# Kernel tuning notes

Measured on AMD Instinct MI355X. Metric: run time of the kernel, lower is better.

The kernel has to match this reference:

```python
import jax, jax.numpy as jnp
import numpy as np
import math

QUERY_DIM = 1024
KEY_DIM = 768
VALUE_DIM = 768
NUM_HEADS = 16
HEAD_DIM = QUERY_DIM // NUM_HEADS


def setup_inputs() -> dict:
    key = jax.random.key(0)
    ks = jax.random.split(key, 11)
    B, Sq, Skv = 4, 2048, 2048
    query = jax.random.normal(ks[0], (B, Sq, QUERY_DIM), dtype=jnp.float32)
    k_in = jax.random.normal(ks[1], (B, Skv, KEY_DIM), dtype=jnp.float32)
    v_in = jax.random.normal(ks[2], (B, Skv, VALUE_DIM), dtype=jnp.float32)
    # Linear weights stored as [in, out] (y = x @ W + b), equivalent to torch's x @ W^T.
    def lin(k, fan_in, fan_out):
        bound = 1.0 / math.sqrt(fan_in)
        kw, kb = jax.random.split(k)
        W = jax.random.uniform(kw, (fan_in, fan_out), minval=-bound, maxval=bound, dtype=jnp.float32)
        b = jax.random.uniform(kb, (fan_out,), minval=-bound, maxval=bound, dtype=jnp.float32)
        return W, b
    Wq, bq = lin(ks[3], QUERY_DIM, QUERY_DIM)
    Wk, bk = lin(ks[4], KEY_DIM, QUERY_DIM)
    Wv, bv = lin(ks[5], VALUE_DIM, QUERY_DIM)
    Wo, bo = lin(ks[6], QUERY_DIM, QUERY_DIM)
    return {"query": query, "key": k_in, "value": v_in,
            "Wq": Wq, "bq": bq, "Wk": Wk, "bk": bk,
            "Wv": Wv, "bv": bv, "Wo": Wo, "bo": bo}


def reference(query, key, value, Wq, bq, Wk, bk, Wv, bv, Wo, bo):
    B, Sq, _ = query.shape
    H, D = NUM_HEADS, HEAD_DIM
    # Projections -> [B, H, S, D]
    Q = (query @ Wq + bq).reshape(B, Sq, H, D).transpose(0, 2, 1, 3)
    K = (key @ Wk + bk).reshape(B, -1, H, D).transpose(0, 2, 1, 3)
    V = (value @ Wv + bv).reshape(B, -1, H, D).transpose(0, 2, 1, 3)
    scale = 1.0 / math.sqrt(D)
    scores = jnp.einsum('bhqd,bhkd->bhqk', Q, K) * scale  # [B,H,Sq,Skv]
    weights = jax.nn.softmax(scores, axis=-1)
    attended = jnp.einsum('bhqk,bhkd->bhqd', weights, V)
    attended = attended.transpose(0, 2, 1, 3).reshape(B, Sq, H * D)
    # torch .squeeze(1): no-op since Sq > 1
    return attended @ Wo + bo
```

## Files before the change

kernel.cpp:

```cpp
#include <hip/hip_runtime.h>

#define B_ 4
#define SQ 2048
#define SKV 2048
#define DMODEL 1024
#define DKV 768
#define NH 16
#define DH 64

typedef unsigned short u16;
typedef __bf16 bf16x4 __attribute__((ext_vector_type(4)));
typedef __bf16 bf16x8 __attribute__((ext_vector_type(8)));
typedef float f32x4 __attribute__((ext_vector_type(4)));
typedef float f32x16 __attribute__((ext_vector_type(16)));

__device__ __forceinline__ u16 f2bf(float f) {
  union { __bf16 b; u16 u; } cv;
  cv.b = (__bf16)f;
  return cv.u;
}

__device__ __forceinline__ unsigned cvtpk(float lo, float hi) {
  unsigned r;
  asm("v_cvt_pk_bf16_f32 %0, %1, %2" : "=v"(r) : "v"(lo), "v"(hi));
  return r;
}

__device__ __forceinline__ float fexp2(float x) {
  float r;
  asm("v_exp_f32 %0, %1" : "=v"(r) : "v"(x));
  return r;
}

#define GLDS(gp, lp) __builtin_amdgcn_global_load_lds(                         \
    (const __attribute__((address_space(1))) unsigned*)(gp),                   \
    (__attribute__((address_space(3))) unsigned*)(lp), 16, 0, 0)


__global__ __launch_bounds__(256)
void wt4_kernel(const float* __restrict__ W0, const float* __restrict__ W1,
                const float* __restrict__ W2, const float* __restrict__ W3,
                u16* __restrict__ T0, u16* __restrict__ T1,
                u16* __restrict__ T2, u16* __restrict__ T3) {
  const int z = blockIdx.z;
  const float* W = (z == 0) ? W0 : (z == 1) ? W1 : (z == 2) ? W2 : W3;
  u16* T = (z == 0) ? T0 : (z == 1) ? T1 : (z == 2) ? T2 : T3;
  const int K = (z == 1 || z == 2) ? DKV : DMODEL;
  const int N = DMODEL;
  int n0 = blockIdx.x * 32, k0 = blockIdx.y * 32;
  if (k0 >= K) return;
  __shared__ float tl[32][33];
  int tx = threadIdx.x, ty = threadIdx.y;
#pragma unroll
  for (int p = 0; p < 4; ++p)
    tl[ty + 8 * p][tx] = W[(size_t)(k0 + ty + 8 * p) * N + n0 + tx];
  __syncthreads();
#pragma unroll
  for (int p = 0; p < 4; ++p) {
    int n = n0 + ty + 8 * p;
    int kx = (k0 + tx) ^ ((n & 7) << 3);
    T[(size_t)n * K + kx] = f2bf(tl[tx][ty + 8 * p]);
  }
}

__global__ __launch_bounds__(256)
void qkv_kernel(const float* __restrict__ Aq, const float* __restrict__ Ak,
                const float* __restrict__ Av,
                const u16* __restrict__ Wtq, const u16* __restrict__ Wtk,
                const u16* __restrict__ Wtv,
                const float* __restrict__ bq, const float* __restrict__ bk,
                const float* __restrict__ bv,
                float sclq,
                u16* __restrict__ Qp, u16* __restrict__ Kp, u16* __restrict__ Vt) {
  __shared__ __align__(16) u16 Alds[128][88];
  __shared__ __align__(16) u16 Blds[128][64];
  const int z = blockIdx.z;
  const float* Af = (z == 0) ? Aq : (z == 1) ? Ak : Av;
  const u16* Wt = (z == 0) ? Wtq : (z == 1) ? Wtk : Wtv;
  const float* bias = (z == 0) ? bq : (z == 1) ? bk : bv;
  const int K = (z == 0) ? DMODEL : DKV;
  const float oscale = (z == 0) ? sclq : 1.0f;

  const int t = threadIdx.x;
  const int l = t & 63;
  const int lx = l & 15, lg = l >> 4;
  const int wid = t >> 6;
  const int wr = wid >> 1, wc = wid & 1;

  int flat = blockIdx.y * 8 + blockIdx.x;
  int by = (flat & 7) * 8 + ((flat >> 3) & 7);
  int bx = flat >> 6;
  const int m0 = by * 128, n0 = bx * 128;

  const int srow = l >> 3;
  const int scol = (l & 7) * 8;
  const int bswz = (lx & 7) << 3;

  f32x4 acc[4][4];
#pragma unroll
  for (int i = 0; i < 4; ++i)
#pragma unroll
    for (int j = 0; j < 4; ++j) acc[i][j] = (f32x4){0.f, 0.f, 0.f, 0.f};

  const int arow = t >> 4;
  const int acol = (t & 15) * 4;
  const float* abase = Af + (size_t)(m0 + arow) * K + acol;

  float4 areg[8];
#pragma unroll
  for (int p = 0; p < 8; ++p)
    areg[p] = *(const float4*)(abase + (size_t)p * 16 * K);

  for (int k0 = 0; k0 < K; k0 += 64) {
    __syncthreads();
#pragma unroll
    for (int j = 0; j < 4; ++j) {
      int row = wid * 32 + j * 8;
      GLDS(Wt + (size_t)(n0 + row + srow) * K + k0 + scol, &Blds[row][0]);
    }
#pragma unroll
    for (int p = 0; p < 8; ++p) {
      union { bf16x4 v; uint2 u; } cv;
      cv.v[0] = (__bf16)areg[p].x; cv.v[1] = (__bf16)areg[p].y;
      cv.v[2] = (__bf16)areg[p].z; cv.v[3] = (__bf16)areg[p].w;
      *(uint2*)(&Alds[p * 16 + arow][acol]) = cv.u;
    }
    __syncthreads();
    if ((k0 + 64) < K) {
#pragma unroll
      for (int p = 0; p < 8; ++p)
        areg[p] = *(const float4*)(abase + (size_t)p * 16 * K + k0 + 64);
    }
#pragma unroll
    for (int kk = 0; kk < 64; kk += 32) {
      bf16x8 af[4], bfr[4];
#pragma unroll
      for (int i = 0; i < 4; ++i)
        af[i] = *(const bf16x8*)(&Alds[wr * 64 + i * 16 + lx][kk + lg * 8]);
#pragma unroll
      for (int j = 0; j < 4; ++j)
        bfr[j] = *(const bf16x8*)(&Blds[wc * 64 + j * 16 + lx][(kk + lg * 8) ^ bswz]);
#pragma unroll
      for (int i = 0; i < 4; ++i)
#pragma unroll
        for (int j = 0; j < 4; ++j)
          acc[i][j] = __builtin_amdgcn_mfma_f32_16x16x32_bf16(af[i], bfr[j], acc[i][j], 0, 0, 0);
    }
  }
#pragma unroll
  for (int j = 0; j < 4; ++j) {
    int col = n0 + wc * 64 + j * 16 + lx;
    float bv = bias[col];
#pragma unroll
    for (int i = 0; i < 4; ++i) {
      int rowb = m0 + wr * 64 + i * 16 + lg * 4;
      f32x4 c = acc[i][j];
      if (z == 2) {
        int b = rowb >> 11, s = rowb & 2047;
        int h = col >> 6, d = col & 63;
        u16* vt = Vt + (size_t)((b * NH + h) * DH + d) * SKV + s;
        union { bf16x4 v; uint2 u; } cv;
        cv.v[0] = (__bf16)(c[0] + bv); cv.v[1] = (__bf16)(c[1] + bv);
        cv.v[2] = (__bf16)(c[2] + bv); cv.v[3] = (__bf16)(c[3] + bv);
        *(uint2*)vt = cv.u;
      } else {
        u16* op = (z == 0) ? Qp : Kp;
#pragma unroll
        for (int r = 0; r < 4; ++r)
          op[(size_t)(rowb + r) * DMODEL + col] = f2bf((c[r] + bv) * oscale);
      }
    }
  }
}

__global__ __launch_bounds__(256)
void oproj_kernel(const u16* __restrict__ Ab, const u16* __restrict__ Wt,
                  const float* __restrict__ bias, float* __restrict__ out_) {
  const int N = DMODEL, K = DMODEL;
  __shared__ __align__(16) u16 Alds[128][64];
  __shared__ __align__(16) u16 Blds[128][64];
  const int t = threadIdx.x;
  const int l = t & 63;
  const int lx = l & 15, lg = l >> 4;
  const int wid = t >> 6;
  const int wr = wid >> 1, wc = wid & 1;

  int flat = blockIdx.y * 8 + blockIdx.x;
  int by = (flat & 7) * 8 + ((flat >> 3) & 7);
  int bx = flat >> 6;
  const int m0 = by * 128, n0 = bx * 128;

  const int srow = l >> 3;
  const int scol = (l & 7) * 8;
  const int swz = (lx & 7) << 3;

  f32x4 acc[4][4];
#pragma unroll
  for (int i = 0; i < 4; ++i)
#pragma unroll
    for (int j = 0; j < 4; ++j) acc[i][j] = (f32x4){0.f, 0.f, 0.f, 0.f};

  for (int k0 = 0; k0 < K; k0 += 64) {
    __syncthreads();
#pragma unroll
    for (int j = 0; j < 4; ++j) {
      int row = wid * 32 + j * 8;
      GLDS(Wt + (size_t)(n0 + row + srow) * K + k0 + scol, &Blds[row][0]);
      GLDS(Ab + (size_t)(m0 + row + srow) * K + k0 + scol, &Alds[row][0]);
    }
    __syncthreads();
#pragma unroll
    for (int kk = 0; kk < 64; kk += 32) {
      bf16x8 af[4], bfr[4];
#pragma unroll
      for (int i = 0; i < 4; ++i)
        af[i] = *(const bf16x8*)(&Alds[wr * 64 + i * 16 + lx][(kk + lg * 8) ^ swz]);
#pragma unroll
      for (int j = 0; j < 4; ++j)
        bfr[j] = *(const bf16x8*)(&Blds[wc * 64 + j * 16 + lx][(kk + lg * 8) ^ swz]);
#pragma unroll
      for (int i = 0; i < 4; ++i)
#pragma unroll
        for (int j = 0; j < 4; ++j)
          acc[i][j] = __builtin_amdgcn_mfma_f32_16x16x32_bf16(af[i], bfr[j], acc[i][j], 0, 0, 0);
    }
  }
#pragma unroll
  for (int j = 0; j < 4; ++j) {
    int col = n0 + wc * 64 + j * 16 + lx;
    float bv = bias[col];
#pragma unroll
    for (int i = 0; i < 4; ++i) {
      int rowb = m0 + wr * 64 + i * 16 + lg * 4;
      f32x4 c = acc[i][j];
#pragma unroll
      for (int r = 0; r < 4; ++r)
        out_[(size_t)(rowb + r) * N + col] = c[r] + bv;
    }
  }
}

#define KVB 128
#define KP 72
#define VP 136

__device__ __forceinline__ void pv_tile(const f32x16& stt, int base,
                                        const u16 (*Vl)[VP], int ql, int hi,
                                        bf16x8 ones, f32x16& a0, f32x16& a1, f32x16& sa) {
  unsigned pk[8];
#pragma unroll
  for (int j = 0; j < 8; ++j) pk[j] = cvtpk(stt[2 * j], stt[2 * j + 1]);
#pragma unroll
  for (int ksl = 0; ksl < 2; ++ksl) {
    auto wA = __builtin_amdgcn_permlane32_swap(pk[4 * ksl + 0], pk[4 * ksl + 2], false, false);
    auto wB = __builtin_amdgcn_permlane32_swap(pk[4 * ksl + 1], pk[4 * ksl + 3], false, false);
    union { unsigned w[4]; bf16x8 v; } pfr;
    pfr.w[0] = (unsigned)wA[0]; pfr.w[1] = (unsigned)wB[0];
    pfr.w[2] = (unsigned)wA[1]; pfr.w[3] = (unsigned)wB[1];
    int ks = base + ksl;
    bf16x8 v0 = *(const bf16x8*)(&Vl[ql][ks * 16 + hi * 8]);
    bf16x8 v1 = *(const bf16x8*)(&Vl[32 + ql][ks * 16 + hi * 8]);
    a0 = __builtin_amdgcn_mfma_f32_32x32x16_bf16(v0, pfr.v, a0, 0, 0, 0);
    a1 = __builtin_amdgcn_mfma_f32_32x32x16_bf16(v1, pfr.v, a1, 0, 0, 0);
    sa = __builtin_amdgcn_mfma_f32_32x32x16_bf16(ones, pfr.v, sa, 0, 0, 0);
  }
}

__global__ __launch_bounds__(512)
void attn_kernel(const u16* __restrict__ Qp, const u16* __restrict__ Kp,
                 const u16* __restrict__ Vt, u16* __restrict__ Att) {
  __shared__ __align__(16) u16 Klds[2][KVB][KP];
  __shared__ __align__(16) u16 Vlds[2][DH][VP];
  const int t = threadIdx.x;
  const int l = t & 63;
  const int ql = l & 31, hi = l >> 5;
  const int wid = t >> 6;

  const int flat = blockIdx.y * 8 + blockIdx.x;
  const int xcd = flat & 7;
  const int rest = flat >> 3;
  const int bh = xcd * 8 + (rest & 7);
  const int qb = rest >> 3;
  const int b = bh >> 4, h = bh & 15;
  const int q = qb * 256 + wid * 32 + ql;

  bf16x8 qf[4];
  const u16* qbase = Qp + (size_t)(b * SQ + q) * DMODEL + h * 64 + hi * 8;
#pragma unroll
  for (int ds = 0; ds < 4; ++ds) qf[ds] = *(const bf16x8*)(qbase + ds * 16);

  bf16x8 ones;
  {
    union { unsigned u[4]; bf16x8 v; } o;
    o.u[0] = o.u[1] = o.u[2] = o.u[3] = 0x3F803F80u;
    ones = o.v;
  }
  f32x16 z16;
#pragma unroll
  for (int r = 0; r < 16; ++r) z16[r] = 0.f;

  f32x16 acc0, acc1, sacc;
#pragma unroll
  for (int r = 0; r < 16; ++r) { acc0[r] = 0.f; acc1[r] = 0.f; sacc[r] = 0.f; }

  const int sr = t >> 3;
  const int sc = (t & 7) * 8;
  const u16* kg = Kp + (size_t)(b * SKV) * DMODEL + h * 64;
  const u16* vg = Vt + ((size_t)(b * NH + h) * DH + sr) * SKV;

  {
    *(uint4*)(&Klds[0][sr][sc])      = *(const uint4*)(kg + (size_t)sr * DMODEL + sc);
    *(uint4*)(&Klds[0][64 + sr][sc]) = *(const uint4*)(kg + (size_t)(64 + sr) * DMODEL + sc);
    *(uint4*)(&Vlds[0][sr][sc])      = *(const uint4*)(vg + sc);
    *(uint4*)(&Vlds[0][sr][64 + sc]) = *(const uint4*)(vg + 64 + sc);
  }
  int cur = 0;

  for (int kv0 = 0; kv0 < SKV; kv0 += KVB) {
    uint4 kr0, kr1, vr0, vr1;
    const bool pf = (kv0 + KVB) < SKV;
    if (pf) {
      kr0 = *(const uint4*)(kg + (size_t)(kv0 + KVB + sr) * DMODEL + sc);
      kr1 = *(const uint4*)(kg + (size_t)(kv0 + KVB + 64 + sr) * DMODEL + sc);
      vr0 = *(const uint4*)(vg + kv0 + KVB + sc);
      vr1 = *(const uint4*)(vg + kv0 + KVB + 64 + sc);
    }
    __syncthreads();

    f32x16 st0, st1, st2, st3;
    __builtin_amdgcn_s_setprio(1);
    {
      bf16x8 k0 = *(const bf16x8*)(&Klds[cur][ql][hi * 8]);
      bf16x8 k1 = *(const bf16x8*)(&Klds[cur][32 + ql][hi * 8]);
      bf16x8 k2 = *(const bf16x8*)(&Klds[cur][64 + ql][hi * 8]);
      bf16x8 k3 = *(const bf16x8*)(&Klds[cur][96 + ql][hi * 8]);
      st0 = __builtin_amdgcn_mfma_f32_32x32x16_bf16(k0, qf[0], z16, 0, 0, 0);
      st1 = __builtin_amdgcn_mfma_f32_32x32x16_bf16(k1, qf[0], z16, 0, 0, 0);
      st2 = __builtin_amdgcn_mfma_f32_32x32x16_bf16(k2, qf[0], z16, 0, 0, 0);
      st3 = __builtin_amdgcn_mfma_f32_32x32x16_bf16(k3, qf[0], z16, 0, 0, 0);
    }
#pragma unroll
    for (int ds = 1; ds < 4; ++ds) {
      bf16x8 k0 = *(const bf16x8*)(&Klds[cur][ql][ds * 16 + hi * 8]);
      bf16x8 k1 = *(const bf16x8*)(&Klds[cur][32 + ql][ds * 16 + hi * 8]);
      bf16x8 k2 = *(const bf16x8*)(&Klds[cur][64 + ql][ds * 16 + hi * 8]);
      bf16x8 k3 = *(const bf16x8*)(&Klds[cur][96 + ql][ds * 16 + hi * 8]);
      st0 = __builtin_amdgcn_mfma_f32_32x32x16_bf16(k0, qf[ds], st0, 0, 0, 0);
      st1 = __builtin_amdgcn_mfma_f32_32x32x16_bf16(k1, qf[ds], st1, 0, 0, 0);
      st2 = __builtin_amdgcn_mfma_f32_32x32x16_bf16(k2, qf[ds], st2, 0, 0, 0);
      st3 = __builtin_amdgcn_mfma_f32_32x32x16_bf16(k3, qf[ds], st3, 0, 0, 0);
    }
    __builtin_amdgcn_s_setprio(0);

#pragma unroll
    for (int r = 0; r < 16; ++r) {
      st0[r] = fexp2(st0[r]); st1[r] = fexp2(st1[r]);
      st2[r] = fexp2(st2[r]); st3[r] = fexp2(st3[r]);
    }

    __builtin_amdgcn_s_setprio(1);
    pv_tile(st0, 0, Vlds[cur], ql, hi, ones, acc0, acc1, sacc);
    pv_tile(st1, 2, Vlds[cur], ql, hi, ones, acc0, acc1, sacc);
    pv_tile(st2, 4, Vlds[cur], ql, hi, ones, acc0, acc1, sacc);
    pv_tile(st3, 6, Vlds[cur], ql, hi, ones, acc0, acc1, sacc);
    __builtin_amdgcn_s_setprio(0);

    if (pf) {
      int nxt = cur ^ 1;
      *(uint4*)(&Klds[nxt][sr][sc])      = kr0;
      *(uint4*)(&Klds[nxt][64 + sr][sc]) = kr1;
      *(uint4*)(&Vlds[nxt][sr][sc])      = vr0;
      *(uint4*)(&Vlds[nxt][sr][64 + sc]) = vr1;
    }
    cur ^= 1;
  }

  float inv = 1.0f / sacc[0];
  u16* ob = Att + (size_t)(b * SQ + q) * DMODEL + h * 64;
  const int oswz = (ql & 7) << 3;
#pragma unroll
  for (int dt = 0; dt < 2; ++dt) {
    const f32x16& a = dt ? acc1 : acc0;
#pragma unroll
    for (int g = 0; g < 4; ++g) {
      unsigned w0 = cvtpk(a[4 * g] * inv, a[4 * g + 1] * inv);
      unsigned w1 = cvtpk(a[4 * g + 2] * inv, a[4 * g + 3] * inv);
      *(uint2*)(ob + ((dt * 32 + g * 8 + hi * 4) ^ oswz)) = make_uint2(w0, w1);
    }
  }
}

extern "C" void kernel_launch(void* const* d_in, const int* in_sizes, int n_in,
                              void* d_out, int out_size, void* d_ws, size_t ws_size,
                              hipStream_t stream) {
  const float* query = (const float*)d_in[0];
  const float* key   = (const float*)d_in[1];
  const float* value = (const float*)d_in[2];
  const float* Wq = (const float*)d_in[3];
  const float* bq = (const float*)d_in[4];
  const float* Wk = (const float*)d_in[5];
  const float* bk = (const float*)d_in[6];
  const float* Wv = (const float*)d_in[7];
  const float* bv = (const float*)d_in[8];
  const float* Wo = (const float*)d_in[9];
  const float* bo = (const float*)d_in[10];
  float* out = (float*)d_out;

  u16* ws = (u16*)d_ws;
  const size_t MTOK = (size_t)B_ * SQ;
  u16* Qp  = ws;
  u16* Kp  = Qp + MTOK * DMODEL;
  u16* Vtb = Kp + MTOK * DMODEL;
  u16* Att = Vtb + MTOK * DMODEL;
  u16* WqT = Att + MTOK * DMODEL;
  u16* WkT = WqT + (size_t)DMODEL * DMODEL;
  u16* WvT = WkT + (size_t)DKV * DMODEL;
  u16* WoT = WvT + (size_t)DKV * DMODEL;

  const float SCL = 0.18033688011112042f;

  dim3 tb(32, 8);
  wt4_kernel<<<dim3(DMODEL / 32, DMODEL / 32, 4), tb, 0, stream>>>(
      Wq, Wk, Wv, Wo, WqT, WkT, WvT, WoT);

  qkv_kernel<<<dim3(DMODEL / 128, MTOK / 128, 3), 256, 0, stream>>>(
      query, key, value, WqT, WkT, WvT, bq, bk, bv, SCL, Qp, Kp, Vtb);

  attn_kernel<<<dim3(SQ / 256, B_ * NH), 512, 0, stream>>>(Qp, Kp, Vtb, Att);

  oproj_kernel<<<dim3(DMODEL / 128, MTOK / 128), 256, 0, stream>>>(Att, WoT, bo, out);
}
```

Before: 177.8 us.

## Pre-cast QKV activations to swizzled bf16 and load A tiles via global_load_lds

```diff
diff --git a/kernel.cpp b/kernel.cpp
--- a/kernel.cpp
+++ b/kernel.cpp
@@ -36,6 +36,29 @@
     (const __attribute__((address_space(1))) unsigned*)(gp),                   \
     (__attribute__((address_space(3))) unsigned*)(lp), 16, 0, 0)
 
+
+__global__ __launch_bounds__(128)
+void cast3_kernel(const float* __restrict__ Aq, const float* __restrict__ Ak,
+                  const float* __restrict__ Av,
+                  u16* __restrict__ Qb, u16* __restrict__ Kb, u16* __restrict__ Vb) {
+  const int z = blockIdx.y;
+  const float* src = (z == 0) ? Aq : (z == 1) ? Ak : Av;
+  u16* dst = (z == 0) ? Qb : (z == 1) ? Kb : Vb;
+  const int K = (z == 0) ? DMODEL : DKV;
+  const int row = blockIdx.x;
+  const int c8 = threadIdx.x * 8;
+  if (c8 >= K) return;
+  const float* s = src + (size_t)row * K + c8;
+  float4 v0 = *(const float4*)s;
+  float4 v1 = *(const float4*)(s + 4);
+  union { bf16x4 b[2]; uint4 u; } cv;
+  cv.b[0][0] = (__bf16)v0.x; cv.b[0][1] = (__bf16)v0.y;
+  cv.b[0][2] = (__bf16)v0.z; cv.b[0][3] = (__bf16)v0.w;
+  cv.b[1][0] = (__bf16)v1.x; cv.b[1][1] = (__bf16)v1.y;
+  cv.b[1][2] = (__bf16)v1.z; cv.b[1][3] = (__bf16)v1.w;
+  int kx = c8 ^ ((row & 7) << 3);
+  *(uint4*)(dst + (size_t)row * K + kx) = cv.u;
+}
 
 __global__ __launch_bounds__(256)
 void wt4_kernel(const float* __restrict__ W0, const float* __restrict__ W1,
@@ -64,18 +87,18 @@
 }
 
 __global__ __launch_bounds__(256)
-void qkv_kernel(const float* __restrict__ Aq, const float* __restrict__ Ak,
-                const float* __restrict__ Av,
+void qkv_kernel(const u16* __restrict__ Qbf, const u16* __restrict__ Kbf,
+                const u16* __restrict__ Vbf,
                 const u16* __restrict__ Wtq, const u16* __restrict__ Wtk,
                 const u16* __restrict__ Wtv,
                 const float* __restrict__ bq, const float* __restrict__ bk,
                 const float* __restrict__ bv,
                 float sclq,
                 u16* __restrict__ Qp, u16* __restrict__ Kp, u16* __restrict__ Vt) {
-  __shared__ __align__(16) u16 Alds[128][88];
+  __shared__ __align__(16) u16 Alds[128][64];
   __shared__ __align__(16) u16 Blds[128][64];
   const int z = blockIdx.z;
-  const float* Af = (z == 0) ? Aq : (z == 1) ? Ak : Av;
+  const u16* Ab = (z == 0) ? Qbf : (z == 1) ? Kbf : Vbf;
   const u16* Wt = (z == 0) ? Wtq : (z == 1) ? Wtk : Wtv;
   const float* bias = (z == 0) ? bq : (z == 1) ? bk : bv;
   const int K = (z == 0) ? DMODEL : DKV;
@@ -94,22 +117,13 @@
 
   const int srow = l >> 3;
   const int scol = (l & 7) * 8;
-  const int bswz = (lx & 7) << 3;
+  const int swz = (lx & 7) << 3;
 
   f32x4 acc[4][4];
 #pragma unroll
   for (int i = 0; i < 4; ++i)
 #pragma unroll
     for (int j = 0; j < 4; ++j) acc[i][j] = (f32x4){0.f, 0.f, 0.f, 0.f};
-
-  const int arow = t >> 4;
-  const int acol = (t & 15) * 4;
-  const float* abase = Af + (size_t)(m0 + arow) * K + acol;
-
-  float4 areg[8];
-#pragma unroll
-  for (int p = 0; p < 8; ++p)
-    areg[p] = *(const float4*)(abase + (size_t)p * 16 * K);
 
   for (int k0 = 0; k0 < K; k0 += 64) {
     __syncthreads();
@@ -117,29 +131,18 @@
     for (int j = 0; j < 4; ++j) {
       int row = wid * 32 + j * 8;
       GLDS(Wt + (size_t)(n0 + row + srow) * K + k0 + scol, &Blds[row][0]);
-    }
-#pragma unroll
-    for (int p = 0; p < 8; ++p) {
-      union { bf16x4 v; uint2 u; } cv;
-      cv.v[0] = (__bf16)areg[p].x; cv.v[1] = (__bf16)areg[p].y;
-      cv.v[2] = (__bf16)areg[p].z; cv.v[3] = (__bf16)areg[p].w;
-      *(uint2*)(&Alds[p * 16 + arow][acol]) = cv.u;
+      GLDS(Ab + (size_t)(m0 + row + srow) * K + k0 + scol, &Alds[row][0]);
     }
     __syncthreads();
-    if ((k0 + 64) < K) {
-#pragma unroll
-      for (int p = 0; p < 8; ++p)
-        areg[p] = *(const float4*)(abase + (size_t)p * 16 * K + k0 + 64);
-    }
 #pragma unroll
     for (int kk = 0; kk < 64; kk += 32) {
       bf16x8 af[4], bfr[4];
 #pragma unroll
       for (int i = 0; i < 4; ++i)
-        af[i] = *(const bf16x8*)(&Alds[wr * 64 + i * 16 + lx][kk + lg * 8]);
+        af[i] = *(const bf16x8*)(&Alds[wr * 64 + i * 16 + lx][(kk + lg * 8) ^ swz]);
 #pragma unroll
       for (int j = 0; j < 4; ++j)
-        bfr[j] = *(const bf16x8*)(&Blds[wc * 64 + j * 16 + lx][(kk + lg * 8) ^ bswz]);
+        bfr[j] = *(const bf16x8*)(&Blds[wc * 64 + j * 16 + lx][(kk + lg * 8) ^ swz]);
 #pragma unroll
       for (int i = 0; i < 4; ++i)
 #pragma unroll
@@ -416,15 +419,20 @@
   u16* WkT = WqT + (size_t)DMODEL * DMODEL;
   u16* WvT = WkT + (size_t)DKV * DMODEL;
   u16* WoT = WvT + (size_t)DKV * DMODEL;
+  u16* Qbf = Att;
+  u16* Kbf = WoT + (size_t)DMODEL * DMODEL;
+  u16* Vbf = Kbf + MTOK * DKV;
 
   const float SCL = 0.18033688011112042f;
+
+  cast3_kernel<<<dim3(MTOK, 3), 128, 0, stream>>>(query, key, value, Qbf, Kbf, Vbf);
 
   dim3 tb(32, 8);
   wt4_kernel<<<dim3(DMODEL / 32, DMODEL / 32, 4), tb, 0, stream>>>(
       Wq, Wk, Wv, Wo, WqT, WkT, WvT, WoT);
 
   qkv_kernel<<<dim3(DMODEL / 128, MTOK / 128, 3), 256, 0, stream>>>(
-      query, key, value, WqT, WkT, WvT, bq, bk, bv, SCL, Qp, Kp, Vtb);
+      Qbf, Kbf, Vbf, WqT, WkT, WvT, bq, bk, bv, SCL, Qp, Kp, Vtb);
 
   attn_kernel<<<dim3(SQ / 256, B_ * NH), 512, 0, stream>>>(Qp, Kp, Vtb, Att);
 
```

After: 186.5 us. 4.9% more time.

## Load QKV A-operand directly into MFMA registers and double-buffer weight tiles

Applied to the files above, without the earlier changes.

```diff
diff --git a/kernel.cpp b/kernel.cpp
--- a/kernel.cpp
+++ b/kernel.cpp
@@ -30,6 +30,15 @@
   float r;
   asm("v_exp_f32 %0, %1" : "=v"(r) : "v"(x));
   return r;
+}
+
+__device__ __forceinline__ bf16x8 cvt8(float4 a, float4 b) {
+  union { bf16x8 v; bf16x4 h[2]; } u;
+  u.h[0][0] = (__bf16)a.x; u.h[0][1] = (__bf16)a.y;
+  u.h[0][2] = (__bf16)a.z; u.h[0][3] = (__bf16)a.w;
+  u.h[1][0] = (__bf16)b.x; u.h[1][1] = (__bf16)b.y;
+  u.h[1][2] = (__bf16)b.z; u.h[1][3] = (__bf16)b.w;
+  return u.v;
 }
 
 #define GLDS(gp, lp) __builtin_amdgcn_global_load_lds(                         \
@@ -72,8 +81,7 @@
                 const float* __restrict__ bv,
                 float sclq,
                 u16* __restrict__ Qp, u16* __restrict__ Kp, u16* __restrict__ Vt) {
-  __shared__ __align__(16) u16 Alds[128][88];
-  __shared__ __align__(16) u16 Blds[128][64];
+  __shared__ __align__(16) u16 Blds[2][128][64];
   const int z = blockIdx.z;
   const float* Af = (z == 0) ? Aq : (z == 1) ? Ak : Av;
   const u16* Wt = (z == 0) ? Wtq : (z == 1) ? Wtk : Wtv;
@@ -94,7 +102,7 @@
 
   const int srow = l >> 3;
   const int scol = (l & 7) * 8;
-  const int bswz = (lx & 7) << 3;
+  const int swz = (lx & 7) << 3;
 
   f32x4 acc[4][4];
 #pragma unroll
@@ -102,51 +110,63 @@
 #pragma unroll
     for (int j = 0; j < 4; ++j) acc[i][j] = (f32x4){0.f, 0.f, 0.f, 0.f};
 
-  const int arow = t >> 4;
-  const int acol = (t & 15) * 4;
-  const float* abase = Af + (size_t)(m0 + arow) * K + acol;
-
-  float4 areg[8];
-#pragma unroll
-  for (int p = 0; p < 8; ++p)
-    areg[p] = *(const float4*)(abase + (size_t)p * 16 * K);
+  const float* ap[4];
+#pragma unroll
+  for (int i = 0; i < 4; ++i)
+    ap[i] = Af + (size_t)(m0 + wr * 64 + i * 16 + lx) * K + lg * 8;
+
+  float4 areg[4][2][2];
+#pragma unroll
+  for (int i = 0; i < 4; ++i)
+#pragma unroll
+    for (int c = 0; c < 2; ++c)
+#pragma unroll
+      for (int h = 0; h < 2; ++h)
+        areg[i][c][h] = *(const float4*)(ap[i] + c * 32 + h * 4);
+
+#pragma unroll
+  for (int j = 0; j < 4; ++j) {
+    int row = wid * 32 + j * 8;
+    GLDS(Wt + (size_t)(n0 + row + srow) * K + scol, &Blds[0][row][0]);
+  }
+  int cur = 0;
 
   for (int k0 = 0; k0 < K; k0 += 64) {
+    const bool pf = (k0 + 64) < K;
     __syncthreads();
-#pragma unroll
-    for (int j = 0; j < 4; ++j) {
-      int row = wid * 32 + j * 8;
-      GLDS(Wt + (size_t)(n0 + row + srow) * K + k0 + scol, &Blds[row][0]);
-    }
-#pragma unroll
-    for (int p = 0; p < 8; ++p) {
-      union { bf16x4 v; uint2 u; } cv;
-      cv.v[0] = (__bf16)areg[p].x; cv.v[1] = (__bf16)areg[p].y;
-      cv.v[2] = (__bf16)areg[p].z; cv.v[3] = (__bf16)areg[p].w;
-      *(uint2*)(&Alds[p * 16 + arow][acol]) = cv.u;
-    }
-    __syncthreads();
-    if ((k0 + 64) < K) {
-#pragma unroll
-      for (int p = 0; p < 8; ++p)
-        areg[p] = *(const float4*)(abase + (size_t)p * 16 * K + k0 + 64);
-    }
-#pragma unroll
-    for (int kk = 0; kk < 64; kk += 32) {
-      bf16x8 af[4], bfr[4];
+    if (pf) {
+#pragma unroll
+      for (int j = 0; j < 4; ++j) {
+        int row = wid * 32 + j * 8;
+        GLDS(Wt + (size_t)(n0 + row + srow) * K + k0 + 64 + scol, &Blds[cur ^ 1][row][0]);
+      }
+    }
+#pragma unroll
+    for (int c = 0; c < 2; ++c) {
+      bf16x8 af[4];
 #pragma unroll
       for (int i = 0; i < 4; ++i)
-        af[i] = *(const bf16x8*)(&Alds[wr * 64 + i * 16 + lx][kk + lg * 8]);
+        af[i] = cvt8(areg[i][c][0], areg[i][c][1]);
+      if (pf) {
+#pragma unroll
+        for (int i = 0; i < 4; ++i)
+#pragma unroll
+          for (int h = 0; h < 2; ++h)
+            areg[i][c][h] = *(const float4*)(ap[i] + k0 + 64 + c * 32 + h * 4);
+      }
+      bf16x8 bfr[4];
 #pragma unroll
       for (int j = 0; j < 4; ++j)
-        bfr[j] = *(const bf16x8*)(&Blds[wc * 64 + j * 16 + lx][(kk + lg * 8) ^ bswz]);
+        bfr[j] = *(const bf16x8*)(&Blds[cur][wc * 64 + j * 16 + lx][(c * 32 + lg * 8) ^ swz]);
 #pragma unroll
       for (int i = 0; i < 4; ++i)
 #pragma unroll
         for (int j = 0; j < 4; ++j)
           acc[i][j] = __builtin_amdgcn_mfma_f32_16x16x32_bf16(af[i], bfr[j], acc[i][j], 0, 0, 0);
     }
-  }
+    cur ^= 1;
+  }
+
 #pragma unroll
   for (int j = 0; j < 4; ++j) {
     int col = n0 + wc * 64 + j * 16 + lx;
```

Result: slower. 270.8 us (+52.3%).

## Double-buffer LDS tiles in QKV projection GEMM to drop a barrier

Applied to the files above, without the earlier changes.

```diff
diff --git a/kernel.cpp b/kernel.cpp
--- a/kernel.cpp
+++ b/kernel.cpp
@@ -72,8 +72,8 @@
                 const float* __restrict__ bv,
                 float sclq,
                 u16* __restrict__ Qp, u16* __restrict__ Kp, u16* __restrict__ Vt) {
-  __shared__ __align__(16) u16 Alds[128][88];
-  __shared__ __align__(16) u16 Blds[128][64];
+  __shared__ __align__(16) u16 Alds[2][128][72];
+  __shared__ __align__(16) u16 Blds[2][128][64];
   const int z = blockIdx.z;
   const float* Af = (z == 0) ? Aq : (z == 1) ? Ak : Av;
   const u16* Wt = (z == 0) ? Wtq : (z == 1) ? Wtk : Wtv;
@@ -111,42 +111,66 @@
   for (int p = 0; p < 8; ++p)
     areg[p] = *(const float4*)(abase + (size_t)p * 16 * K);
 
+#pragma unroll
+  for (int p = 0; p < 8; ++p) {
+    union { bf16x4 v; uint2 u; } cv;
+    cv.v[0] = (__bf16)areg[p].x; cv.v[1] = (__bf16)areg[p].y;
+    cv.v[2] = (__bf16)areg[p].z; cv.v[3] = (__bf16)areg[p].w;
+    *(uint2*)(&Alds[0][p * 16 + arow][acol]) = cv.u;
+  }
+#pragma unroll
+  for (int j = 0; j < 4; ++j) {
+    int row = wid * 32 + j * 8;
+    GLDS(Wt + (size_t)(n0 + row + srow) * K + scol, &Blds[0][row][0]);
+  }
+  if (64 < K) {
+#pragma unroll
+    for (int p = 0; p < 8; ++p)
+      areg[p] = *(const float4*)(abase + (size_t)p * 16 * K + 64);
+  }
+
+  int cur = 0;
   for (int k0 = 0; k0 < K; k0 += 64) {
+    const bool pf = (k0 + 64) < K;
+    const bool pf2 = (k0 + 128) < K;
     __syncthreads();
-#pragma unroll
-    for (int j = 0; j < 4; ++j) {
-      int row = wid * 32 + j * 8;
-      GLDS(Wt + (size_t)(n0 + row + srow) * K + k0 + scol, &Blds[row][0]);
-    }
-#pragma unroll
-    for (int p = 0; p < 8; ++p) {
-      union { bf16x4 v; uint2 u; } cv;
-      cv.v[0] = (__bf16)areg[p].x; cv.v[1] = (__bf16)areg[p].y;
-      cv.v[2] = (__bf16)areg[p].z; cv.v[3] = (__bf16)areg[p].w;
-      *(uint2*)(&Alds[p * 16 + arow][acol]) = cv.u;
-    }
-    __syncthreads();
-    if ((k0 + 64) < K) {
+    if (pf) {
+#pragma unroll
+      for (int j = 0; j < 4; ++j) {
+        int row = wid * 32 + j * 8;
+        GLDS(Wt + (size_t)(n0 + row + srow) * K + k0 + 64 + scol, &Blds[cur ^ 1][row][0]);
+      }
+#pragma unroll
+      for (int p = 0; p < 8; ++p) {
+        union { bf16x4 v; uint2 u; } cv;
+        cv.v[0] = (__bf16)areg[p].x; cv.v[1] = (__bf16)areg[p].y;
+        cv.v[2] = (__bf16)areg[p].z; cv.v[3] = (__bf16)areg[p].w;
+        *(uint2*)(&Alds[cur ^ 1][p * 16 + arow][acol]) = cv.u;
+      }
+    }
+    if (pf2) {
 #pragma unroll
       for (int p = 0; p < 8; ++p)
-        areg[p] = *(const float4*)(abase + (size_t)p * 16 * K + k0 + 64);
+        areg[p] = *(const float4*)(abase + (size_t)p * 16 * K + k0 + 128);
     }
 #pragma unroll
     for (int kk = 0; kk < 64; kk += 32) {
       bf16x8 af[4], bfr[4];
 #pragma unroll
       for (int i = 0; i < 4; ++i)
-        af[i] = *(const bf16x8*)(&Alds[wr * 64 + i * 16 + lx][kk + lg * 8]);
+        af[i] = *(const bf16x8*)(&Alds[cur][wr * 64 + i * 16 + lx][kk + lg * 8]);
 #pragma unroll
       for (int j = 0; j < 4; ++j)
-        bfr[j] = *(const bf16x8*)(&Blds[wc * 64 + j * 16 + lx][(kk + lg * 8) ^ bswz]);
+        bfr[j] = *(const bf16x8*)(&Blds[cur][wc * 64 + j * 16 + lx][(kk + lg * 8) ^ bswz]);
 #pragma unroll
       for (int i = 0; i < 4; ++i)
 #pragma unroll
         for (int j = 0; j < 4; ++j)
           acc[i][j] = __builtin_amdgcn_mfma_f32_16x16x32_bf16(af[i], bfr[j], acc[i][j], 0, 0, 0);
     }
-  }
+    cur ^= 1;
+  }
+
 #pragma unroll
   for (int j = 0; j < 4; ++j) {
     int col = n0 + wc * 64 + j * 16 + lx;
```

Measured after the change: 176.0 us, median of 3. No clear change (-1.0%).
